# Kernel tuning notes

Measured on AMD Instinct MI355X. Metric: run time of the kernel, lower is better.

The kernel has to match this reference:

```python
import jax, jax.numpy as jnp
import numpy as np

B, H, S, D = 4, 16, 2048, 128


def setup_inputs() -> dict:
    key0 = jax.random.key(0)
    kq, kk, kv, km = jax.random.split(key0, 4)
    query = jax.random.normal(kq, (B, H, S, D), dtype=jnp.float32)
    key = jax.random.normal(kk, (B, H, S, D), dtype=jnp.float32)
    value = jax.random.normal(kv, (B, H, S, D), dtype=jnp.float32)
    mask = jax.random.normal(km, (1, 1, S, S), dtype=jnp.float32)
    return {"query": query, "key": key, "value": value, "mask": mask}


def reference(query, key, value, mask):
    # qk: [B, H, S, S]
    qk = jnp.einsum('bhqd,bhkd->bhqk', query, key)
    qk = qk + mask
    # NOTE: original module divides by sqrt(D) AFTER adding the mask
    scale = 1.0 / jnp.sqrt(jnp.asarray(key.shape[-1], dtype=query.dtype))
    attn = jax.nn.softmax(qk * scale, axis=-1)
    return jnp.einsum('bhqk,bhkd->bhqd', attn, value)
```

## Files before the change

kernel.cpp:

```cpp
#include <hip/hip_runtime.h>
#include <math.h>

#define SEQ   2048
#define HD    128
#define KVB   64
#define NT    (SEQ / KVB)
#define SCALE_L2E 0.12753242193263556f

typedef __bf16 bf16_t;
typedef __bf16 bf16x2 __attribute__((ext_vector_type(2)));
typedef __bf16 bf16x4 __attribute__((ext_vector_type(4)));
typedef __bf16 bf16x8 __attribute__((ext_vector_type(8)));
typedef float  f32x16 __attribute__((ext_vector_type(16)));

__device__ __forceinline__ void gl_lds16(const void* g, void* l) {
  __builtin_amdgcn_global_load_lds(
      (const __attribute__((address_space(1))) unsigned int*)g,
      (__attribute__((address_space(3))) unsigned int*)l, 16, 0, 0);
}

__global__ __launch_bounds__(256)
void mk_kimg(const float* __restrict__ k, char* __restrict__ img) {
  const int bt = blockIdx.x;
  const float* src = k + (size_t)bt * KVB * HD;
  char* dst = img + (size_t)bt * 16384;
  const int tid = threadIdx.x;
#pragma unroll
  for (int i = 0; i < 8; ++i) {
    const int g = tid + i * 256;
    const int r = g >> 5, c4 = g & 31;
    float4 v = *(const float4*)(src + (size_t)r * HD + c4 * 4);
    const int o = (r * 256 + c4 * 8) ^ ((r & 7) << 4);
    *(bf16x4*)(dst + o) = bf16x4{(bf16_t)v.x, (bf16_t)v.y, (bf16_t)v.z, (bf16_t)v.w};
  }
}

__global__ __launch_bounds__(256)
void mk_vimg(const float* __restrict__ v, char* __restrict__ img) {
  __shared__ float tile[KVB][HD + 4];
  const int bt = blockIdx.x;
  const float* src = v + (size_t)bt * KVB * HD;
  char* dst = img + (size_t)bt * 16384;
  const int tid = threadIdx.x;
#pragma unroll
  for (int i = 0; i < 8; ++i) {
    const int g = tid + i * 256;
    const int r = g >> 5, c4 = g & 31;
    float4 a = *(const float4*)(src + (size_t)r * HD + c4 * 4);
    tile[r][c4 * 4 + 0] = a.x; tile[r][c4 * 4 + 1] = a.y;
    tile[r][c4 * 4 + 2] = a.z; tile[r][c4 * 4 + 3] = a.w;
  }
  __syncthreads();
#pragma unroll
  for (int i = 0; i < 8; ++i) {
    const int g = tid + i * 256;
    const int o = g * 8;
    const int d = o >> 7;
    const int inner = (o & 127) ^ ((d & 7) << 4);
    const int pe0 = inner >> 1;
    bf16x4 w;
#pragma unroll
    for (int e = 0; e < 4; ++e) {
      const int pe = pe0 + e;
      const int a  = pe >> 4;
      const int bp = pe & 15;
      const int vv = bp >> 1;
      const int sv = (vv & 1) | ((vv & 2) << 1) | ((vv & 4) >> 1);
      const int kk = a * 16 + sv * 2 + (bp & 1);
      w[e] = (bf16_t)tile[kk][d];
    }
    *(bf16x4*)(dst + o) = w;
  }
}

__global__ __launch_bounds__(256)
void mask_tr2(const float* __restrict__ m, bf16x2* __restrict__ mt2) {
  __shared__ float tile[32][65];
  const int tid = threadIdx.x;
  const int k0  = blockIdx.x * 64;
  const int q0  = blockIdx.y * 32;
#pragma unroll
  for (int i = 0; i < 2; ++i) {
    const int ix = tid + i * 256;
    const int qr = ix >> 4, c4 = ix & 15;
    float4 v = *(const float4*)(m + (size_t)(q0 + qr) * SEQ + k0 + c4 * 4);
    tile[qr][c4 * 4 + 0] = v.x; tile[qr][c4 * 4 + 1] = v.y;
    tile[qr][c4 * 4 + 2] = v.z; tile[qr][c4 * 4 + 3] = v.w;
  }
  __syncthreads();
#pragma unroll
  for (int i = 0; i < 4; ++i) {
    const int ix = tid + i * 256;
    const int kl = ix >> 5, qq = ix & 31;
    mt2[(size_t)(blockIdx.x * 32 + kl) * SEQ + q0 + qq] =
        bf16x2{(bf16_t)(tile[qq][kl] * SCALE_L2E),
               (bf16_t)(tile[qq][kl + 32] * SCALE_L2E)};
  }
}

__global__ __launch_bounds__(256)
void mask_tr(const float* __restrict__ m, float* __restrict__ mt) {
  __shared__ float tile[32][33];
  const int tx = threadIdx.x & 31;
  const int ty = threadIdx.x >> 5;
  const int kb = blockIdx.x * 32;
  const int qb = blockIdx.y * 32;
#pragma unroll
  for (int r = 0; r < 32; r += 8)
    tile[ty + r][tx] = m[(size_t)(qb + ty + r) * SEQ + kb + tx] * SCALE_L2E;
  __syncthreads();
#pragma unroll
  for (int r = 0; r < 32; r += 8)
    mt[(size_t)(kb + ty + r) * SEQ + qb + tx] = tile[tx][ty + r];
}

__global__ __launch_bounds__(256, 2)
void attn_fwd_v6(const float* __restrict__ q_g, const char* __restrict__ kimg,
                 const char* __restrict__ vimg, const bf16x2* __restrict__ mt2_g,
                 float* __restrict__ o_g) {
  __shared__ __align__(16) char ldsK[KVB * 256];
  __shared__ __align__(16) char ldsV[2][HD * 128];

  const int tid  = threadIdx.x;
  const int wid  = tid >> 6;
  const int lane = tid & 63;
  const int hi   = lane >> 5;
  const int ql   = lane & 31;

  const int lin = blockIdx.x;
  const int xcd = lin & 7;
  const int idx = lin >> 3;
  const int bh  = xcd + 8 * (idx >> 4);
  const int q0  = (idx & 15) * 128;

  const float* Qb = q_g + (size_t)bh * SEQ * HD;
  float*       Ob = o_g + (size_t)bh * SEQ * HD;

  const int qrow = q0 + wid * 32 + ql;

  bf16x8 qf[8];
#pragma unroll
  for (int kd = 0; kd < 8; ++kd) {
    const float* p = Qb + (size_t)qrow * HD + kd * 16 + hi * 8;
    float4 a = *(const float4*)p;
    float4 b = *(const float4*)(p + 4);
    qf[kd] = bf16x8{(bf16_t)a.x, (bf16_t)a.y, (bf16_t)a.z, (bf16_t)a.w,
                    (bf16_t)b.x, (bf16_t)b.y, (bf16_t)b.z, (bf16_t)b.w};
  }

  f32x16 ot[4];
#pragma unroll
  for (int dt = 0; dt < 4; ++dt)
#pragma unroll
    for (int r = 0; r < 16; ++r) ot[dt][r] = 0.f;

  f32x16 lsum;
#pragma unroll
  for (int r = 0; r < 16; ++r) lsum[r] = 0.f;

#define STAGE_K(T)                                                           \
  { const char* gK = kimg + ((size_t)bh * NT + (T)) * 16384 + wid * 4096 +   \
                     lane * 16;                                              \
    char* lK = ldsK + wid * 4096;                                            \
    _Pragma("unroll") for (int j = 0; j < 4; ++j)                            \
      gl_lds16(gK + j * 1024, lK + j * 1024); }

#define STAGE_V(T, BUF)                                                      \
  { const char* gV = vimg + ((size_t)bh * NT + (T)) * 16384 + wid * 4096 +   \
                     lane * 16;                                              \
    char* lV = ldsV[BUF] + wid * 4096;                                       \
    _Pragma("unroll") for (int j = 0; j < 4; ++j)                            \
      gl_lds16(gV + j * 1024, lV + j * 1024); }

  STAGE_K(0)
  STAGE_V(0, 0)

  for (int t = 0; t < NT; ++t) {
    __syncthreads();
    const int vbuf = t & 1;
    const char* Vl = ldsV[vbuf];
    const bool more = (t + 1 < NT);

    bf16x2 mreg[16];
    {
      const bf16x2* MTp = mt2_g + (size_t)(t * 32) * SEQ + qrow;
#pragma unroll
      for (int r = 0; r < 16; ++r) {
        const int kl = (r & 3) + 8 * (r >> 2) + 4 * hi;
        mreg[r] = MTp[(size_t)kl * SEQ];
      }
    }

    if (more) { STAGE_V(t + 1, vbuf ^ 1) }

    f32x16 s0, s1;
#pragma unroll
    for (int r = 0; r < 16; ++r) { s0[r] = 0.f; s1[r] = 0.f; }
#pragma unroll
    for (int kd = 0; kd < 8; ++kd) {
      int b0 = ql * 256 + kd * 32 + hi * 16; b0 ^= (ql & 7) << 4;
      bf16x8 kf0 = *(const bf16x8*)(ldsK + b0);
      bf16x8 kf1 = *(const bf16x8*)(ldsK + b0 + 8192);
      s0 = __builtin_amdgcn_mfma_f32_32x32x16_bf16(kf0, qf[kd], s0, 0, 0, 0);
      s1 = __builtin_amdgcn_mfma_f32_32x32x16_bf16(kf1, qf[kd], s1, 0, 0, 0);
    }

    __syncthreads();

    if (more) { STAGE_K(t + 1) }

    float p0[16], p1[16];
#pragma unroll
    for (int r = 0; r < 16; ++r) {
      p0[r] = __builtin_amdgcn_exp2f(fmaf(s0[r], SCALE_L2E, (float)mreg[r][0]));
      p1[r] = __builtin_amdgcn_exp2f(fmaf(s1[r], SCALE_L2E, (float)mreg[r][1]));
    }
#pragma unroll
    for (int r = 0; r < 16; ++r) lsum[r] += p0[r] + p1[r];

    bf16x8 pb[2][2];
#pragma unroll
    for (int kf = 0; kf < 2; ++kf) {
      pb[0][kf] = bf16x8{(bf16_t)p0[8*kf+0], (bf16_t)p0[8*kf+1],
                         (bf16_t)p0[8*kf+2], (bf16_t)p0[8*kf+3],
                         (bf16_t)p0[8*kf+4], (bf16_t)p0[8*kf+5],
                         (bf16_t)p0[8*kf+6], (bf16_t)p0[8*kf+7]};
      pb[1][kf] = bf16x8{(bf16_t)p1[8*kf+0], (bf16_t)p1[8*kf+1],
                         (bf16_t)p1[8*kf+2], (bf16_t)p1[8*kf+3],
                         (bf16_t)p1[8*kf+4], (bf16_t)p1[8*kf+5],
                         (bf16_t)p1[8*kf+6], (bf16_t)p1[8*kf+7]};
    }

#pragma unroll
    for (int tt = 0; tt < 2; ++tt)
#pragma unroll
      for (int kf = 0; kf < 2; ++kf) {
        const int kg = tt * 2 + kf;
#pragma unroll
        for (int dt = 0; dt < 4; ++dt) {
          const int d = dt * 32 + ql;
          int byt = d * 128 + kg * 32 + hi * 16; byt ^= (d & 7) << 4;
          bf16x8 vf = *(const bf16x8*)(Vl + byt);
          ot[dt] = __builtin_amdgcn_mfma_f32_32x32x16_bf16(vf, pb[tt][kf], ot[dt], 0, 0, 0);
        }
      }
  }

  float ls[16];
#pragma unroll
  for (int r = 0; r < 16; ++r) ls[r] = lsum[r];
#pragma unroll
  for (int off = 8; off > 0; off >>= 1)
#pragma unroll
    for (int r = 0; r < off; ++r) ls[r] += ls[r + off];
  const float l_run = ls[0] + __shfl_xor(ls[0], 32, 64);

  const float rinv = 1.f / l_run;
  float* Op = Ob + (size_t)qrow * HD;
#pragma unroll
  for (int dt = 0; dt < 4; ++dt)
#pragma unroll
    for (int r = 0; r < 16; ++r) {
      const int d = dt * 32 + (r & 3) + 8 * (r >> 2) + 4 * hi;
      Op[d] = ot[dt][r] * rinv;
    }
}

__global__ __launch_bounds__(256, 2)
void attn_fwd_fb(const float* __restrict__ q_g, const float* __restrict__ k_g,
                 const float* __restrict__ v_g, const float* __restrict__ mt_g,
                 float* __restrict__ o_g) {
  __shared__ __align__(16) char ldsK[2][KVB * 256];
  __shared__ __align__(16) char ldsV[2][HD * 128];

  const int tid  = threadIdx.x;
  const int wid  = tid >> 6;
  const int lane = tid & 63;
  const int hi   = lane >> 5;
  const int ql   = lane & 31;

  const int lin = blockIdx.x;
  const int xcd = lin & 7;
  const int idx = lin >> 3;
  const int bh  = xcd + 8 * (idx >> 4);
  const int q0  = (idx & 15) * 128;

  const float* Qb = q_g + (size_t)bh * SEQ * HD;
  const float* Kb = k_g + (size_t)bh * SEQ * HD;
  const float* Vb = v_g + (size_t)bh * SEQ * HD;
  float*       Ob = o_g + (size_t)bh * SEQ * HD;

  const int qrow = q0 + wid * 32 + ql;

  bf16x8 qf[8];
#pragma unroll
  for (int kd = 0; kd < 8; ++kd) {
    const float* p = Qb + (size_t)qrow * HD + kd * 16 + hi * 8;
    float4 a = *(const float4*)p;
    float4 b = *(const float4*)(p + 4);
    qf[kd] = bf16x8{(bf16_t)a.x, (bf16_t)a.y, (bf16_t)a.z, (bf16_t)a.w,
                    (bf16_t)b.x, (bf16_t)b.y, (bf16_t)b.z, (bf16_t)b.w};
  }

  f32x16 ot[4];
#pragma unroll
  for (int dt = 0; dt < 4; ++dt)
#pragma unroll
    for (int r = 0; r < 16; ++r) ot[dt][r] = 0.f;

  float m_run = -INFINITY, l_run = 0.f;

  float4 kreg[8], vA[4], vB[4];
  const int vp  = tid & 31;
  const int vcb = tid >> 5;
  const int vkb = ((vp >> 3) << 5) +
                  (((vp & 1) | ((vp & 2) << 1) | ((vp & 4) >> 1)) << 2);

#define KF_ISSUE(K0)                                                         \
  { _Pragma("unroll") for (int i = 0; i < 8; ++i) {                          \
      const int ix = tid + i * 256;                                          \
      kreg[i] = *(const float4*)(Kb + (size_t)((K0) + (ix >> 5)) * HD +      \
                                 (ix & 31) * 4); } }

#define KF_WRITE(BUF)                                                        \
  { char* dK = ldsK[BUF];                                                    \
    _Pragma("unroll") for (int i = 0; i < 8; ++i) {                          \
      const int ix = tid + i * 256;                                          \
      const int row = ix >> 5; const int c4 = ix & 31;                       \
      int byt = row * 256 + c4 * 8; byt ^= (row & 7) << 4;                   \
      float4 v = kreg[i];                                                    \
      *(bf16x4*)(dK + byt) =                                                 \
          bf16x4{(bf16_t)v.x, (bf16_t)v.y, (bf16_t)v.z, (bf16_t)v.w}; } }

#define VF_ISSUE_A(K0)                                                       \
  { _Pragma("unroll") for (int i = 0; i < 2; ++i) {                          \
      const int c4 = vcb + 8 * i;                                            \
      vA[2*i]   = *(const float4*)(Vb + (size_t)((K0) + 2*vp)     * HD + c4*4); \
      vA[2*i+1] = *(const float4*)(Vb + (size_t)((K0) + 2*vp + 1) * HD + c4*4); } }

#define VF_ISSUE_B(K0)                                                       \
  { _Pragma("unroll") for (int i = 0; i < 2; ++i) {                          \
      const int c4 = vcb + 16 + 8 * i;                                       \
      vB[2*i]   = *(const float4*)(Vb + (size_t)((K0) + 2*vp)     * HD + c4*4); \
      vB[2*i+1] = *(const float4*)(Vb + (size_t)((K0) + 2*vp + 1) * HD + c4*4); } }

#define VF_WRITE_X(BUF, REGS, COFF)                                          \
  { char* dV = ldsV[BUF];                                                    \
    _Pragma("unroll") for (int i = 0; i < 2; ++i) {                          \
      const int c4 = vcb + (COFF) + 8 * i;                                   \
      const float* r0 = (const float*)&REGS[2*i];                            \
      const float* r1 = (const float*)&REGS[2*i+1];                          \
      _Pragma("unroll") for (int j = 0; j < 4; ++j) {                        \
        const int d = c4 * 4 + j;                                            \
        int byt = d * 128 + vkb; byt ^= (d & 7) << 4;                        \
        *(bf16x2*)(dV + byt) = bf16x2{(bf16_t)r0[j], (bf16_t)r1[j]}; } } }

  KF_ISSUE(0)
  VF_ISSUE_A(0)
  VF_ISSUE_B(0)
  KF_WRITE(0)
  VF_WRITE_X(0, vA, 0)
  VF_WRITE_X(0, vB, 16)

  for (int t = 0; t < NT; ++t) {
    __syncthreads();
    const int buf = t & 1;
    const char* Kl = ldsK[buf];
    const char* Vl = ldsV[buf];
    const bool more = (t + 1 < NT);

    if (more) { KF_ISSUE((t + 1) * KVB) }

    float mk0[16], mk1[16];
    {
      const float* MTp = mt_g + (size_t)(t * KVB) * SEQ + qrow;
#pragma unroll
      for (int r = 0; r < 16; ++r) {
        const int k = (r & 3) + 8 * (r >> 2) + 4 * hi;
        mk0[r] = MTp[(size_t)k * SEQ];
        mk1[r] = MTp[(size_t)(k + 32) * SEQ];
      }
    }

    if (more) { VF_ISSUE_A((t + 1) * KVB) }

    f32x16 s0, s1;
#pragma unroll
    for (int r = 0; r < 16; ++r) { s0[r] = 0.f; s1[r] = 0.f; }
#pragma unroll
    for (int kd = 0; kd < 8; ++kd) {
      int b0 = ql * 256 + kd * 32 + hi * 16; b0 ^= (ql & 7) << 4;
      bf16x8 kf0 = *(const bf16x8*)(Kl + b0);
      bf16x8 kf1 = *(const bf16x8*)(Kl + b0 + 8192);
      s0 = __builtin_amdgcn_mfma_f32_32x32x16_bf16(kf0, qf[kd], s0, 0, 0, 0);
      s1 = __builtin_amdgcn_mfma_f32_32x32x16_bf16(kf1, qf[kd], s1, 0, 0, 0);
    }

    if (more) {
      VF_WRITE_X(buf ^ 1, vA, 0)
      VF_ISSUE_B((t + 1) * KVB)
    }

    float x0[16], x1[16];
#pragma unroll
    for (int r = 0; r < 16; ++r) {
      x0[r] = fmaf(s0[r], SCALE_L2E, mk0[r]);
      x1[r] = fmaf(s1[r], SCALE_L2E, mk1[r]);
    }
    float tm[16];
#pragma unroll
    for (int r = 0; r < 16; ++r) tm[r] = fmaxf(x0[r], x1[r]);
#pragma unroll
    for (int off = 8; off > 0; off >>= 1)
#pragma unroll
      for (int r = 0; r < off; ++r) tm[r] = fmaxf(tm[r], tm[r + off]);
    const float mx   = fmaxf(tm[0], __shfl_xor(tm[0], 32, 64));
    const float mnew = fmaxf(m_run, mx);
    const float fac  = __builtin_amdgcn_exp2f(m_run - mnew);
    m_run = mnew;

    float p0[16], p1[16];
#pragma unroll
    for (int r = 0; r < 16; ++r) {
      p0[r] = __builtin_amdgcn_exp2f(x0[r] - mnew);
      p1[r] = __builtin_amdgcn_exp2f(x1[r] - mnew);
    }
    float ts[16];
#pragma unroll
    for (int r = 0; r < 16; ++r) ts[r] = p0[r] + p1[r];
#pragma unroll
    for (int off = 8; off > 0; off >>= 1)
#pragma unroll
      for (int r = 0; r < off; ++r) ts[r] += ts[r + off];
    const float sum = ts[0] + __shfl_xor(ts[0], 32, 64);
    l_run = l_run * fac + sum;

#pragma unroll
    for (int dt = 0; dt < 4; ++dt)
#pragma unroll
      for (int r = 0; r < 16; ++r) ot[dt][r] *= fac;

    bf16x8 pb[2][2];
#pragma unroll
    for (int kf = 0; kf < 2; ++kf) {
      pb[0][kf] = bf16x8{(bf16_t)p0[8*kf+0], (bf16_t)p0[8*kf+1],
                         (bf16_t)p0[8*kf+2], (bf16_t)p0[8*kf+3],
                         (bf16_t)p0[8*kf+4], (bf16_t)p0[8*kf+5],
                         (bf16_t)p0[8*kf+6], (bf16_t)p0[8*kf+7]};
      pb[1][kf] = bf16x8{(bf16_t)p1[8*kf+0], (bf16_t)p1[8*kf+1],
                         (bf16_t)p1[8*kf+2], (bf16_t)p1[8*kf+3],
                         (bf16_t)p1[8*kf+4], (bf16_t)p1[8*kf+5],
                         (bf16_t)p1[8*kf+6], (bf16_t)p1[8*kf+7]};
    }

#pragma unroll
    for (int tt = 0; tt < 2; ++tt)
#pragma unroll
      for (int kf = 0; kf < 2; ++kf) {
        const int kg = tt * 2 + kf;
#pragma unroll
        for (int dt = 0; dt < 4; ++dt) {
          const int d = dt * 32 + ql;
          int byt = d * 128 + kg * 32 + hi * 16; byt ^= (d & 7) << 4;
          bf16x8 vf = *(const bf16x8*)(Vl + byt);
          ot[dt] = __builtin_amdgcn_mfma_f32_32x32x16_bf16(vf, pb[tt][kf], ot[dt], 0, 0, 0);
        }
      }

    if (more) {
      VF_WRITE_X(buf ^ 1, vB, 16)
      KF_WRITE(buf ^ 1)
    }
  }

  const float rinv = 1.f / l_run;
  float* Op = Ob + (size_t)qrow * HD;
#pragma unroll
  for (int dt = 0; dt < 4; ++dt)
#pragma unroll
    for (int r = 0; r < 16; ++r) {
      const int d = dt * 32 + (r & 3) + 8 * (r >> 2) + 4 * hi;
      Op[d] = ot[dt][r] * rinv;
    }
}

extern "C" void kernel_launch(void* const* d_in, const int* in_sizes, int n_in,
                              void* d_out, int out_size, void* d_ws, size_t ws_size,
                              hipStream_t stream) {
  (void)in_sizes; (void)n_in; (void)out_size;
  const float* Q = (const float*)d_in[0];
  const float* K = (const float*)d_in[1];
  const float* V = (const float*)d_in[2];
  const float* M = (const float*)d_in[3];
  float*       O = (float*)d_out;

  const size_t szImg = (size_t)64 * NT * 16384;
  const size_t szM2  = (size_t)(SEQ / KVB) * 32 * SEQ * 4;

  if (ws_size >= 2 * szImg + szM2) {
    char*   KI  = (char*)d_ws;
    char*   VI  = (char*)d_ws + szImg;
    bf16x2* MT2 = (bf16x2*)((char*)d_ws + 2 * szImg);
    mk_kimg<<<64 * NT, 256, 0, stream>>>(K, KI);
    mk_vimg<<<64 * NT, 256, 0, stream>>>(V, VI);
    mask_tr2<<<dim3(SEQ / 64, SEQ / 32), 256, 0, stream>>>(M, MT2);
    attn_fwd_v6<<<dim3(1024), 256, 0, stream>>>(Q, KI, VI, MT2, O);
  } else {
    float* MT = (float*)d_ws;
    mask_tr<<<dim3(SEQ / 32, SEQ / 32), 256, 0, stream>>>(M, MT);
    attn_fwd_fb<<<dim3(1024), 256, 0, stream>>>(Q, K, V, MT, O);
  }
}
```

Baseline: 216.2 us.

## Software-pipeline attention loop: interleave next QK^T MFMAs with current PV MFMAs

Restructures the attention main loop so the QK^T scores for tile t+1 are computed while the PV product for tile t runs, interleaving the two MFMA streams in one loop body. K becomes double-buffered and V triple-buffered in LDS, staging runs two tiles ahead, and the mask for the next tile is prefetched into registers. This cuts the two barriers per iteration to one and hides exp/softmax latency behind matrix work. In exchange LDS use grows from 48KB to 80KB per block and register pressure rises, which may lower occupancy below the two blocks per CU requested in the launch bounds.

```diff
diff --git a/kernel.cpp b/kernel.cpp
--- a/kernel.cpp
+++ b/kernel.cpp
@@ -115,11 +115,11 @@
 }
 
 __global__ __launch_bounds__(256, 2)
-void attn_fwd_v6(const float* __restrict__ q_g, const char* __restrict__ kimg,
+void attn_fwd_v7(const float* __restrict__ q_g, const char* __restrict__ kimg,
                  const char* __restrict__ vimg, const bf16x2* __restrict__ mt2_g,
                  float* __restrict__ o_g) {
-  __shared__ __align__(16) char ldsK[KVB * 256];
-  __shared__ __align__(16) char ldsV[2][HD * 128];
+  __shared__ __align__(16) char ldsK[2][16384];
+  __shared__ __align__(16) char ldsV[3][16384];
 
   const int tid  = threadIdx.x;
   const int wid  = tid >> 6;
@@ -158,10 +158,10 @@
 #pragma unroll
   for (int r = 0; r < 16; ++r) lsum[r] = 0.f;
 
-#define STAGE_K(T)                                                           \
+#define STAGE_K(T, BUF)                                                      \
   { const char* gK = kimg + ((size_t)bh * NT + (T)) * 16384 + wid * 4096 +   \
                      lane * 16;                                              \
-    char* lK = ldsK + wid * 4096;                                            \
+    char* lK = ldsK[BUF] + wid * 4096;                                       \
     _Pragma("unroll") for (int j = 0; j < 4; ++j)                            \
       gl_lds16(gK + j * 1024, lK + j * 1024); }
 
@@ -172,48 +172,42 @@
     _Pragma("unroll") for (int j = 0; j < 4; ++j)                            \
       gl_lds16(gV + j * 1024, lV + j * 1024); }
 
-  STAGE_K(0)
+#define LOAD_MASK(T)                                                         \
+  { const bf16x2* MTp = mt2_g + (size_t)((T) * 32) * SEQ + qrow;             \
+    _Pragma("unroll") for (int r = 0; r < 16; ++r) {                         \
+      const int kl = (r & 3) + 8 * (r >> 2) + 4 * hi;                        \
+      mcur[r] = MTp[(size_t)kl * SEQ]; } }
+
+  bf16x2 mcur[16];
+
+  STAGE_K(0, 0)
   STAGE_V(0, 0)
-
-  for (int t = 0; t < NT; ++t) {
-    __syncthreads();
-    const int vbuf = t & 1;
-    const char* Vl = ldsV[vbuf];
-    const bool more = (t + 1 < NT);
-
-    bf16x2 mreg[16];
-    {
-      const bf16x2* MTp = mt2_g + (size_t)(t * 32) * SEQ + qrow;
-#pragma unroll
-      for (int r = 0; r < 16; ++r) {
-        const int kl = (r & 3) + 8 * (r >> 2) + 4 * hi;
-        mreg[r] = MTp[(size_t)kl * SEQ];
-      }
-    }
-
-    if (more) { STAGE_V(t + 1, vbuf ^ 1) }
-
-    f32x16 s0, s1;
-#pragma unroll
-    for (int r = 0; r < 16; ++r) { s0[r] = 0.f; s1[r] = 0.f; }
+  LOAD_MASK(0)
+  __syncthreads();
+  STAGE_K(1, 1)
+  STAGE_V(1, 1)
+
+  f32x16 s0, s1;
+#pragma unroll
+  for (int r = 0; r < 16; ++r) { s0[r] = 0.f; s1[r] = 0.f; }
+  {
+    const char* Kl = ldsK[0];
 #pragma unroll
     for (int kd = 0; kd < 8; ++kd) {
       int b0 = ql * 256 + kd * 32 + hi * 16; b0 ^= (ql & 7) << 4;
-      bf16x8 kf0 = *(const bf16x8*)(ldsK + b0);
-      bf16x8 kf1 = *(const bf16x8*)(ldsK + b0 + 8192);
+      bf16x8 kf0 = *(const bf16x8*)(Kl + b0);
+      bf16x8 kf1 = *(const bf16x8*)(Kl + b0 + 8192);
       s0 = __builtin_amdgcn_mfma_f32_32x32x16_bf16(kf0, qf[kd], s0, 0, 0, 0);
       s1 = __builtin_amdgcn_mfma_f32_32x32x16_bf16(kf1, qf[kd], s1, 0, 0, 0);
     }
-
-    __syncthreads();
-
-    if (more) { STAGE_K(t + 1) }
-
+  }
+
+  for (int t = 0; t < NT; ++t) {
     float p0[16], p1[16];
 #pragma unroll
     for (int r = 0; r < 16; ++r) {
-      p0[r] = __builtin_amdgcn_exp2f(fmaf(s0[r], SCALE_L2E, (float)mreg[r][0]));
-      p1[r] = __builtin_amdgcn_exp2f(fmaf(s1[r], SCALE_L2E, (float)mreg[r][1]));
+      p0[r] = __builtin_amdgcn_exp2f(fmaf(s0[r], SCALE_L2E, (float)mcur[r][0]));
+      p1[r] = __builtin_amdgcn_exp2f(fmaf(s1[r], SCALE_L2E, (float)mcur[r][1]));
     }
 #pragma unroll
     for (int r = 0; r < 16; ++r) lsum[r] += p0[r] + p1[r];
@@ -231,19 +225,49 @@
                          (bf16_t)p1[8*kf+6], (bf16_t)p1[8*kf+7]};
     }
 
-#pragma unroll
-    for (int tt = 0; tt < 2; ++tt)
-#pragma unroll
-      for (int kf = 0; kf < 2; ++kf) {
-        const int kg = tt * 2 + kf;
-#pragma unroll
-        for (int dt = 0; dt < 4; ++dt) {
-          const int d = dt * 32 + ql;
+    if (t + 1 < NT) { LOAD_MASK(t + 1) }
+
+    __syncthreads();
+
+    if (t + 2 < NT) {
+      STAGE_K(t + 2, t & 1)
+      STAGE_V(t + 2, (t + 2) % 3)
+    }
+
+    const char* Vl = ldsV[t % 3];
+    if (t + 1 < NT) {
+      const char* Kl = ldsK[(t + 1) & 1];
+#pragma unroll
+      for (int r = 0; r < 16; ++r) { s0[r] = 0.f; s1[r] = 0.f; }
+#pragma unroll
+      for (int kd = 0; kd < 8; ++kd) {
+        int b0 = ql * 256 + kd * 32 + hi * 16; b0 ^= (ql & 7) << 4;
+        bf16x8 kf0 = *(const bf16x8*)(Kl + b0);
+        bf16x8 kf1 = *(const bf16x8*)(Kl + b0 + 8192);
+        s0 = __builtin_amdgcn_mfma_f32_32x32x16_bf16(kf0, qf[kd], s0, 0, 0, 0);
+        s1 = __builtin_amdgcn_mfma_f32_32x32x16_bf16(kf1, qf[kd], s1, 0, 0, 0);
+#pragma unroll
+        for (int u = 0; u < 2; ++u) {
+          const int i  = kd * 2 + u;
+          const int tt = i >> 3, kf = (i >> 2) & 1, dt = i & 3;
+          const int kg = tt * 2 + kf;
+          const int d  = dt * 32 + ql;
           int byt = d * 128 + kg * 32 + hi * 16; byt ^= (d & 7) << 4;
           bf16x8 vf = *(const bf16x8*)(Vl + byt);
           ot[dt] = __builtin_amdgcn_mfma_f32_32x32x16_bf16(vf, pb[tt][kf], ot[dt], 0, 0, 0);
         }
       }
+    } else {
+#pragma unroll
+      for (int i = 0; i < 16; ++i) {
+        const int tt = i >> 3, kf = (i >> 2) & 1, dt = i & 3;
+        const int kg = tt * 2 + kf;
+        const int d  = dt * 32 + ql;
+        int byt = d * 128 + kg * 32 + hi * 16; byt ^= (d & 7) << 4;
+        bf16x8 vf = *(const bf16x8*)(Vl + byt);
+        ot[dt] = __builtin_amdgcn_mfma_f32_32x32x16_bf16(vf, pb[tt][kf], ot[dt], 0, 0, 0);
+      }
+    }
   }
 
   float ls[16];
@@ -504,7 +528,7 @@
     mk_kimg<<<64 * NT, 256, 0, stream>>>(K, KI);
     mk_vimg<<<64 * NT, 256, 0, stream>>>(V, VI);
     mask_tr2<<<dim3(SEQ / 64, SEQ / 32), 256, 0, stream>>>(M, MT2);
-    attn_fwd_v6<<<dim3(1024), 256, 0, stream>>>(Q, KI, VI, MT2, O);
+    attn_fwd_v7<<<dim3(1024), 256, 0, stream>>>(Q, KI, VI, MT2, O);
   } else {
     float* MT = (float*)d_ws;
     mask_tr<<<dim3(SEQ / 32, SEQ / 32), 256, 0, stream>>>(M, MT);
```

New measurement: 230.7 us. 6.7% more time.
